# Optimization experiments

Measured on AMD Instinct MI355X. Metric: run time of the kernel, lower is better.

Reference implementation:

```python
import jax, jax.numpy as jnp
import numpy as np

D_MODEL = 1024
N_HEADS = 16
D_K = D_MODEL // N_HEADS


def setup_inputs() -> dict:
    key = jax.random.key(0)
    ks = jax.random.split(key, 11)
    B, S, D = 2, 2048, D_MODEL
    scale = 1.0 / np.sqrt(D)
    inp = {
        "q": jax.random.normal(ks[0], (B, S, D), jnp.float32),
        "k": jax.random.normal(ks[1], (B, S, D), jnp.float32),
        "v": jax.random.normal(ks[2], (B, S, D), jnp.float32),
        "wq": jax.random.normal(ks[3], (D, D), jnp.float32) * scale,
        "bq": jax.random.normal(ks[4], (D,), jnp.float32) * 0.01,
        "wk": jax.random.normal(ks[5], (D, D), jnp.float32) * scale,
        "bk": jax.random.normal(ks[6], (D,), jnp.float32) * 0.01,
        "wv": jax.random.normal(ks[7], (D, D), jnp.float32) * scale,
        "bv": jax.random.normal(ks[8], (D,), jnp.float32) * 0.01,
        "wo": jax.random.normal(ks[9], (D, D), jnp.float32) * scale,
        "bo": jax.random.normal(ks[10], (D,), jnp.float32) * 0.01,
    }
    return inp


def _split_heads(x, B):
    # [B, S, D] -> [B, H, S, d_k]
    return x.reshape(B, -1, N_HEADS, D_K).transpose(0, 2, 1, 3)


def reference(q, k, v, wq, bq, wk, bk, wv, bv, wo, bo):
    B, S, D = q.shape
    # Linear projections (torch Linear: x @ W^T + b)
    qh = _split_heads(q @ wq.T + bq, B)  # [B,H,S,dk]
    kh = _split_heads(k @ wk.T + bk, B)
    vh = _split_heads(v @ wv.T + bv, B)
    scores = jnp.einsum("bhqd,bhkd->bhqk", qh, kh) / jnp.sqrt(jnp.float32(D_K))
    attn = jax.nn.softmax(scores, axis=-1)  # [B,H,S,S]
    out = jnp.einsum("bhqk,bhkd->bhqd", attn, vh)  # [B,H,S,dk]
    out = out.transpose(0, 2, 1, 3).reshape(B, S, D)
    out = out @ wo.T + bo
    return (out, attn)
```

## Files before the change

### kernel.cpp

```cpp
#include <hip/hip_runtime.h>

#define D_MODEL 1024
#define N_HEADS 16
#define D_K     64
#define BB      2
#define SS      2048
#define M_TOT   (BB * SS)

typedef __attribute__((ext_vector_type(8))) short short8;
typedef __attribute__((ext_vector_type(4))) float f32x4;

__device__ __forceinline__ unsigned short bf_rne(float x) {
    unsigned u = __builtin_bit_cast(unsigned, x);
    u += 0x7fff + ((u >> 16) & 1);
    return (unsigned short)(u >> 16);
}
__device__ __forceinline__ void split2(float x, unsigned short& h, unsigned short& l) {
    unsigned short hh = bf_rne(x);
    float hf = __builtin_bit_cast(float, ((unsigned)hh) << 16);
    l = bf_rne(x - hf);
    h = hh;
}

__device__ __forceinline__ int swz(int r, int k) {
    return r * 64 + ((((k >> 3) ^ (r & 7)) << 3) | (k & 7));
}

__global__ __launch_bounds__(256) void split_f32(
    const float* __restrict__ in, unsigned short* __restrict__ h,
    unsigned short* __restrict__ l, int n4)
{
    int i = blockIdx.x * 256 + threadIdx.x;
    if (i >= n4) return;
    float4 v = ((const float4*)in)[i];
    unsigned short hh[4], ll[4];
    split2(v.x, hh[0], ll[0]); split2(v.y, hh[1], ll[1]);
    split2(v.z, hh[2], ll[2]); split2(v.w, hh[3], ll[3]);
    *(ushort4*)&h[i * 4] = make_ushort4(hh[0], hh[1], hh[2], hh[3]);
    *(ushort4*)&l[i * 4] = make_ushort4(ll[0], ll[1], ll[2], ll[3]);
}

template <int BN, int STORE, bool BIAS>
__global__ __launch_bounds__(256, 2) void gemm3(
    const float* __restrict__ A, long sAz, int lda,
    const unsigned short* __restrict__ Bh, const unsigned short* __restrict__ Bl,
    long sBz, int ldb,
    const float* __restrict__ bias,
    float* __restrict__ Cf, unsigned short* __restrict__ Ch,
    unsigned short* __restrict__ Cl,
    long sCz, int ldc, int K, float scale)
{
    constexpr int NF = (BN == 128) ? 4 : 2;
    constexpr int PB = BN / 32;

    const int z = blockIdx.z;
    A  += (long)z * sAz;
    Bh += (long)z * sBz;
    Bl += (long)z * sBz;

    const int m0 = blockIdx.y * 128;
    const int n0 = blockIdx.x * BN;
    const int t  = threadIdx.x;
    const int lane = t & 63;
    const int wy = t >> 7;
    const int wx = (t >> 6) & 1;

    __shared__ __align__(16) unsigned short Ahs[128 * 64];
    __shared__ __align__(16) unsigned short Als[128 * 64];
    __shared__ __align__(16) unsigned short Bhs[BN * 64];
    __shared__ __align__(16) unsigned short Bls[BN * 64];

    const int sr = t >> 3;
    const int sc = (t & 7) * 8;

    f32x4 acc[4][NF];
#pragma unroll
    for (int i = 0; i < 4; ++i)
#pragma unroll
        for (int j = 0; j < NF; ++j) acc[i][j] = (f32x4){0.f, 0.f, 0.f, 0.f};

    for (int k0 = 0; k0 < K; k0 += 64) {
        float4 a0[4], a1[4];
#pragma unroll
        for (int p = 0; p < 4; ++p) {
            const float* s = &A[(long)(m0 + sr + 32 * p) * lda + k0 + sc];
            a0[p] = *(const float4*)s;
            a1[p] = *(const float4*)(s + 4);
        }
        short8 gbh[PB], gbl[PB];
#pragma unroll
        for (int p = 0; p < PB; ++p) {
            const long bo = (long)(n0 + sr + 32 * p) * ldb + k0 + sc;
            gbh[p] = *(const short8*)&Bh[bo];
            gbl[p] = *(const short8*)&Bl[bo];
        }
        __syncthreads();
#pragma unroll
        for (int p = 0; p < 4; ++p) {
            union { short8 v; unsigned short u[8]; } ph, pl;
            float f[8] = {a0[p].x, a0[p].y, a0[p].z, a0[p].w,
                          a1[p].x, a1[p].y, a1[p].z, a1[p].w};
#pragma unroll
            for (int e = 0; e < 8; ++e) split2(f[e], ph.u[e], pl.u[e]);
            const int idx = swz(sr + 32 * p, sc);
            *(short8*)&Ahs[idx] = ph.v;
            *(short8*)&Als[idx] = pl.v;
        }
#pragma unroll
        for (int p = 0; p < PB; ++p) {
            const int idx = swz(sr + 32 * p, sc);
            *(short8*)&Bhs[idx] = gbh[p];
            *(short8*)&Bls[idx] = gbl[p];
        }
        __syncthreads();

#pragma unroll
        for (int ks = 0; ks < 2; ++ks) {
            const int fr = lane & 15;
            const int fk = ks * 32 + (lane >> 4) * 8;
            short8 ah[4], al[4], bh8[NF], bl8[NF];
#pragma unroll
            for (int i = 0; i < 4; ++i) {
                const int idx = swz(wy * 64 + i * 16 + fr, fk);
                ah[i] = *(const short8*)&Ahs[idx];
                al[i] = *(const short8*)&Als[idx];
            }
#pragma unroll
            for (int j = 0; j < NF; ++j) {
                const int idx = swz(wx * (16 * NF) + j * 16 + fr, fk);
                bh8[j] = *(const short8*)&Bhs[idx];
                bl8[j] = *(const short8*)&Bls[idx];
            }
#pragma unroll
            for (int i = 0; i < 4; ++i)
#pragma unroll
                for (int j = 0; j < NF; ++j) {
                    acc[i][j] = __builtin_amdgcn_mfma_f32_16x16x32_bf16(ah[i], bh8[j], acc[i][j], 0, 0, 0);
                    acc[i][j] = __builtin_amdgcn_mfma_f32_16x16x32_bf16(al[i], bh8[j], acc[i][j], 0, 0, 0);
                    acc[i][j] = __builtin_amdgcn_mfma_f32_16x16x32_bf16(ah[i], bl8[j], acc[i][j], 0, 0, 0);
                    acc[i][j] = __builtin_amdgcn_mfma_f32_16x16x32_bf16(al[i], bl8[j], acc[i][j], 0, 0, 0);
                }
        }
    }

    const int fr = lane & 15;
    const int fq = lane >> 4;
#pragma unroll
    for (int j = 0; j < NF; ++j) {
        const int n = n0 + wx * (16 * NF) + j * 16 + fr;
        const float bj = BIAS ? bias[n] : 0.0f;
#pragma unroll
        for (int i = 0; i < 4; ++i)
#pragma unroll
            for (int r = 0; r < 4; ++r) {
                const int m = m0 + wy * 64 + i * 16 + fq * 4 + r;
                const float val = acc[i][j][r] * scale + bj;
                if (STORE == 0) {
                    Cf[(long)z * sCz + (long)m * ldc + n] = val;
                } else if (STORE == 1) {
                    const int b = m >> 11, s = m & 2047, h = n >> 6, d = n & 63;
                    Cf[(((long)(b * N_HEADS + h)) * SS + s) * 64 + d] = val;
                } else if (STORE == 2) {
                    const int b = m >> 11, s = m & 2047, h = n >> 6, d = n & 63;
                    unsigned short hh, ll; split2(val, hh, ll);
                    const long idx = (((long)(b * N_HEADS + h)) * SS + s) * 64 + d;
                    Ch[idx] = hh; Cl[idx] = ll;
                } else if (STORE == 3) {
                    const int b = m >> 11, s = m & 2047, h = n >> 6, d = n & 63;
                    unsigned short hh, ll; split2(val, hh, ll);
                    const long idx = (((long)(b * N_HEADS + h)) * 64 + d) * SS + s;
                    Ch[idx] = hh; Cl[idx] = ll;
                } else {
                    const int b = z >> 4, h = z & 15;
                    Cf[((long)(b * SS + m)) * D_MODEL + h * 64 + n] = val;
                }
            }
    }
}

__global__ __launch_bounds__(256) void softmax_rows(float* __restrict__ attn)
{
    const long row = blockIdx.x;
    float* p = attn + row * (long)SS;
    const int t = threadIdx.x;

    float4 v0 = *(const float4*)&p[t * 4];
    float4 v1 = *(const float4*)&p[(t + 256) * 4];

    float m = fmaxf(fmaxf(fmaxf(v0.x, v0.y), fmaxf(v0.z, v0.w)),
                    fmaxf(fmaxf(v1.x, v1.y), fmaxf(v1.z, v1.w)));
#pragma unroll
    for (int off = 32; off >= 1; off >>= 1)
        m = fmaxf(m, __shfl_xor(m, off));

    __shared__ float red[8];
    if ((t & 63) == 0) red[t >> 6] = m;
    __syncthreads();
    m = fmaxf(fmaxf(red[0], red[1]), fmaxf(red[2], red[3]));

    v0.x = __expf(v0.x - m); v0.y = __expf(v0.y - m);
    v0.z = __expf(v0.z - m); v0.w = __expf(v0.w - m);
    v1.x = __expf(v1.x - m); v1.y = __expf(v1.y - m);
    v1.z = __expf(v1.z - m); v1.w = __expf(v1.w - m);

    float s = (v0.x + v0.y + v0.z + v0.w) + (v1.x + v1.y + v1.z + v1.w);
#pragma unroll
    for (int off = 32; off >= 1; off >>= 1)
        s += __shfl_xor(s, off);
    if ((t & 63) == 0) red[4 + (t >> 6)] = s;
    __syncthreads();
    s = (red[4] + red[5]) + (red[6] + red[7]);

    const float r = 1.0f / s;
    v0.x *= r; v0.y *= r; v0.z *= r; v0.w *= r;
    v1.x *= r; v1.y *= r; v1.z *= r; v1.w *= r;

    *(float4*)&p[t * 4] = v0;
    *(float4*)&p[(t + 256) * 4] = v1;
}

extern "C" void kernel_launch(void* const* d_in, const int* in_sizes, int n_in,
                              void* d_out, int out_size, void* d_ws, size_t ws_size,
                              hipStream_t stream)
{
    const float* q  = (const float*)d_in[0];
    const float* k  = (const float*)d_in[1];
    const float* v  = (const float*)d_in[2];
    const float* wq = (const float*)d_in[3];
    const float* bq = (const float*)d_in[4];
    const float* wk = (const float*)d_in[5];
    const float* bk = (const float*)d_in[6];
    const float* wv = (const float*)d_in[7];
    const float* bv = (const float*)d_in[8];
    const float* wo = (const float*)d_in[9];
    const float* bo = (const float*)d_in[10];

    float* out  = (float*)d_out;
    float* attn = out + (long)BB * SS * D_MODEL;

    char* ws = (char*)d_ws;
    float*          qh    = (float*)ws;
    unsigned short* kh_hi = (unsigned short*)(ws + (16L << 20));
    unsigned short* kh_lo = (unsigned short*)(ws + (24L << 20));
    unsigned short* vt_hi = (unsigned short*)(ws + (32L << 20));
    unsigned short* vt_lo = (unsigned short*)(ws + (40L << 20));
    float*          oh    = (float*)(ws + (48L << 20));
    unsigned short* wq_hi = (unsigned short*)(ws + (48L << 20));
    unsigned short* wq_lo = (unsigned short*)(ws + (50L << 20));
    unsigned short* wk_hi = (unsigned short*)(ws + (52L << 20));
    unsigned short* wk_lo = (unsigned short*)(ws + (54L << 20));
    unsigned short* wv_hi = (unsigned short*)(ws + (56L << 20));
    unsigned short* wv_lo = (unsigned short*)(ws + (58L << 20));
    unsigned short* wo_hi = (unsigned short*)(ws);
    unsigned short* wo_lo = (unsigned short*)(ws + (2L << 20));

    const dim3 blk(256);
    const int NW4 = (D_MODEL * D_MODEL) / 4;

    hipLaunchKernelGGL(split_f32, dim3(1024), blk, 0, stream, wq, wq_hi, wq_lo, NW4);
    hipLaunchKernelGGL(split_f32, dim3(1024), blk, 0, stream, wk, wk_hi, wk_lo, NW4);
    hipLaunchKernelGGL(split_f32, dim3(1024), blk, 0, stream, wv, wv_hi, wv_lo, NW4);

    const dim3 gproj(D_MODEL / 128, M_TOT / 128, 1);
    hipLaunchKernelGGL((gemm3<128, 1, true>), gproj, blk, 0, stream,
                       q, 0L, D_MODEL, wq_hi, wq_lo, 0L, D_MODEL, bq,
                       qh, (unsigned short*)nullptr, (unsigned short*)nullptr,
                       0L, 0, D_MODEL, 1.0f);
    hipLaunchKernelGGL((gemm3<128, 2, true>), gproj, blk, 0, stream,
                       k, 0L, D_MODEL, wk_hi, wk_lo, 0L, D_MODEL, bk,
                       (float*)nullptr, kh_hi, kh_lo, 0L, 0, D_MODEL, 1.0f);
    hipLaunchKernelGGL((gemm3<128, 3, true>), gproj, blk, 0, stream,
                       v, 0L, D_MODEL, wv_hi, wv_lo, 0L, D_MODEL, bv,
                       (float*)nullptr, vt_hi, vt_lo, 0L, 0, D_MODEL, 1.0f);

    const dim3 gsc(SS / 128, SS / 128, BB * N_HEADS);
    hipLaunchKernelGGL((gemm3<128, 0, false>), gsc, blk, 0, stream,
                       qh, (long)SS * 64, 64, kh_hi, kh_lo, (long)SS * 64, 64,
                       (const float*)nullptr,
                       attn, (unsigned short*)nullptr, (unsigned short*)nullptr,
                       (long)SS * SS, SS, D_K, 0.125f);

    hipLaunchKernelGGL(split_f32, dim3(1024), blk, 0, stream, wo, wo_hi, wo_lo, NW4);

    hipLaunchKernelGGL(softmax_rows, dim3(BB * N_HEADS * SS), blk, 0, stream, attn);

    const dim3 gpv(1, SS / 128, BB * N_HEADS);
    hipLaunchKernelGGL((gemm3<64, 4, false>), gpv, blk, 0, stream,
                       attn, (long)SS * SS, SS, vt_hi, vt_lo, (long)64 * SS, SS,
                       (const float*)nullptr,
                       oh, (unsigned short*)nullptr, (unsigned short*)nullptr,
                       0L, 0, SS, 1.0f);

    hipLaunchKernelGGL((gemm3<128, 0, true>), gproj, blk, 0, stream,
                       oh, 0L, D_MODEL, wo_hi, wo_lo, 0L, D_MODEL, bo,
                       out, (unsigned short*)nullptr, (unsigned short*)nullptr,
                       0L, D_MODEL, D_MODEL, 1.0f);
}
```

Before: 1.248 ms.

## Fuse QK^T, softmax and PV into one attention kernel; drop lo*lo MFMA term

Replaces the separate scores GEMM, row softmax kernel and PV GEMM with one fused kernel per (head, 128-row tile). It first computes scaled scores, writes them raw to the attn output and tracks an online row max and sum. It then re-reads the scores, normalizes them, writes the final probabilities back, and splits them to bf16 hi/lo for the PV MFMAs. Q is now stored as a bf16 hi/lo split, and the lo*lo MFMA term is dropped in all GEMMs, cutting matrix work by a quarter at a small cost in precision. The aim is to save launches and one full pass over the large attention matrix, at the cost of lower parallelism and a sequential two-phase schedule inside each block.

```diff
diff --git a/kernel.cpp b/kernel.cpp
--- a/kernel.cpp
+++ b/kernel.cpp
@@ -40,26 +40,18 @@
     *(ushort4*)&l[i * 4] = make_ushort4(ll[0], ll[1], ll[2], ll[3]);
 }
 
-template <int BN, int STORE, bool BIAS>
+template <int STORE, bool BIAS>
 __global__ __launch_bounds__(256, 2) void gemm3(
-    const float* __restrict__ A, long sAz, int lda,
+    const float* __restrict__ A, int lda,
     const unsigned short* __restrict__ Bh, const unsigned short* __restrict__ Bl,
-    long sBz, int ldb,
+    int ldb,
     const float* __restrict__ bias,
     float* __restrict__ Cf, unsigned short* __restrict__ Ch,
     unsigned short* __restrict__ Cl,
-    long sCz, int ldc, int K, float scale)
+    int ldc, int K)
 {
-    constexpr int NF = (BN == 128) ? 4 : 2;
-    constexpr int PB = BN / 32;
-
-    const int z = blockIdx.z;
-    A  += (long)z * sAz;
-    Bh += (long)z * sBz;
-    Bl += (long)z * sBz;
-
     const int m0 = blockIdx.y * 128;
-    const int n0 = blockIdx.x * BN;
+    const int n0 = blockIdx.x * 128;
     const int t  = threadIdx.x;
     const int lane = t & 63;
     const int wy = t >> 7;
@@ -67,17 +59,17 @@
 
     __shared__ __align__(16) unsigned short Ahs[128 * 64];
     __shared__ __align__(16) unsigned short Als[128 * 64];
-    __shared__ __align__(16) unsigned short Bhs[BN * 64];
-    __shared__ __align__(16) unsigned short Bls[BN * 64];
+    __shared__ __align__(16) unsigned short Bhs[128 * 64];
+    __shared__ __align__(16) unsigned short Bls[128 * 64];
 
     const int sr = t >> 3;
     const int sc = (t & 7) * 8;
 
-    f32x4 acc[4][NF];
+    f32x4 acc[4][4];
 #pragma unroll
     for (int i = 0; i < 4; ++i)
 #pragma unroll
-        for (int j = 0; j < NF; ++j) acc[i][j] = (f32x4){0.f, 0.f, 0.f, 0.f};
+        for (int j = 0; j < 4; ++j) acc[i][j] = (f32x4){0.f, 0.f, 0.f, 0.f};
 
     for (int k0 = 0; k0 < K; k0 += 64) {
         float4 a0[4], a1[4];
@@ -87,9 +79,9 @@
             a0[p] = *(const float4*)s;
             a1[p] = *(const float4*)(s + 4);
         }
-        short8 gbh[PB], gbl[PB];
-#pragma unroll
-        for (int p = 0; p < PB; ++p) {
+        short8 gbh[4], gbl[4];
+#pragma unroll
+        for (int p = 0; p < 4; ++p) {
             const long bo = (long)(n0 + sr + 32 * p) * ldb + k0 + sc;
             gbh[p] = *(const short8*)&Bh[bo];
             gbl[p] = *(const short8*)&Bl[bo];
@@ -105,10 +97,6 @@
             const int idx = swz(sr + 32 * p, sc);
             *(short8*)&Ahs[idx] = ph.v;
             *(short8*)&Als[idx] = pl.v;
-        }
-#pragma unroll
-        for (int p = 0; p < PB; ++p) {
-            const int idx = swz(sr + 32 * p, sc);
             *(short8*)&Bhs[idx] = gbh[p];
             *(short8*)&Bls[idx] = gbl[p];
         }
@@ -118,7 +106,7 @@
         for (int ks = 0; ks < 2; ++ks) {
             const int fr = lane & 15;
             const int fk = ks * 32 + (lane >> 4) * 8;
-            short8 ah[4], al[4], bh8[NF], bl8[NF];
+            short8 ah[4], al[4], bh8[4], bl8[4];
 #pragma unroll
             for (int i = 0; i < 4; ++i) {
                 const int idx = swz(wy * 64 + i * 16 + fr, fk);
@@ -126,19 +114,18 @@
                 al[i] = *(const short8*)&Als[idx];
             }
 #pragma unroll
-            for (int j = 0; j < NF; ++j) {
-                const int idx = swz(wx * (16 * NF) + j * 16 + fr, fk);
+            for (int j = 0; j < 4; ++j) {
+                const int idx = swz(wx * 64 + j * 16 + fr, fk);
                 bh8[j] = *(const short8*)&Bhs[idx];
                 bl8[j] = *(const short8*)&Bls[idx];
             }
 #pragma unroll
             for (int i = 0; i < 4; ++i)
 #pragma unroll
-                for (int j = 0; j < NF; ++j) {
+                for (int j = 0; j < 4; ++j) {
                     acc[i][j] = __builtin_amdgcn_mfma_f32_16x16x32_bf16(ah[i], bh8[j], acc[i][j], 0, 0, 0);
                     acc[i][j] = __builtin_amdgcn_mfma_f32_16x16x32_bf16(al[i], bh8[j], acc[i][j], 0, 0, 0);
                     acc[i][j] = __builtin_amdgcn_mfma_f32_16x16x32_bf16(ah[i], bl8[j], acc[i][j], 0, 0, 0);
-                    acc[i][j] = __builtin_amdgcn_mfma_f32_16x16x32_bf16(al[i], bl8[j], acc[i][j], 0, 0, 0);
                 }
         }
     }
@@ -146,77 +133,274 @@
     const int fr = lane & 15;
     const int fq = lane >> 4;
 #pragma unroll
-    for (int j = 0; j < NF; ++j) {
-        const int n = n0 + wx * (16 * NF) + j * 16 + fr;
+    for (int j = 0; j < 4; ++j) {
+        const int n = n0 + wx * 64 + j * 16 + fr;
         const float bj = BIAS ? bias[n] : 0.0f;
 #pragma unroll
         for (int i = 0; i < 4; ++i)
 #pragma unroll
             for (int r = 0; r < 4; ++r) {
                 const int m = m0 + wy * 64 + i * 16 + fq * 4 + r;
-                const float val = acc[i][j][r] * scale + bj;
+                const float val = acc[i][j][r] + bj;
                 if (STORE == 0) {
-                    Cf[(long)z * sCz + (long)m * ldc + n] = val;
-                } else if (STORE == 1) {
-                    const int b = m >> 11, s = m & 2047, h = n >> 6, d = n & 63;
-                    Cf[(((long)(b * N_HEADS + h)) * SS + s) * 64 + d] = val;
+                    Cf[(long)m * ldc + n] = val;
                 } else if (STORE == 2) {
                     const int b = m >> 11, s = m & 2047, h = n >> 6, d = n & 63;
                     unsigned short hh, ll; split2(val, hh, ll);
                     const long idx = (((long)(b * N_HEADS + h)) * SS + s) * 64 + d;
                     Ch[idx] = hh; Cl[idx] = ll;
-                } else if (STORE == 3) {
+                } else {
                     const int b = m >> 11, s = m & 2047, h = n >> 6, d = n & 63;
                     unsigned short hh, ll; split2(val, hh, ll);
                     const long idx = (((long)(b * N_HEADS + h)) * 64 + d) * SS + s;
                     Ch[idx] = hh; Cl[idx] = ll;
-                } else {
-                    const int b = z >> 4, h = z & 15;
-                    Cf[((long)(b * SS + m)) * D_MODEL + h * 64 + n] = val;
                 }
             }
     }
 }
 
-__global__ __launch_bounds__(256) void softmax_rows(float* __restrict__ attn)
+__global__ __launch_bounds__(256, 2) void attn_fused(
+    const unsigned short* __restrict__ qh_hi, const unsigned short* __restrict__ qh_lo,
+    const unsigned short* __restrict__ kh_hi, const unsigned short* __restrict__ kh_lo,
+    const unsigned short* __restrict__ vt_hi, const unsigned short* __restrict__ vt_lo,
+    float* __restrict__ attn, float* __restrict__ oh)
 {
-    const long row = blockIdx.x;
-    float* p = attn + row * (long)SS;
-    const int t = threadIdx.x;
-
-    float4 v0 = *(const float4*)&p[t * 4];
-    float4 v1 = *(const float4*)&p[(t + 256) * 4];
-
-    float m = fmaxf(fmaxf(fmaxf(v0.x, v0.y), fmaxf(v0.z, v0.w)),
-                    fmaxf(fmaxf(v1.x, v1.y), fmaxf(v1.z, v1.w)));
-#pragma unroll
-    for (int off = 32; off >= 1; off >>= 1)
-        m = fmaxf(m, __shfl_xor(m, off));
-
-    __shared__ float red[8];
-    if ((t & 63) == 0) red[t >> 6] = m;
+    const int z  = blockIdx.x;
+    const int m0 = blockIdx.y * 128;
+    const int b  = z >> 4;
+    const int h  = z & 15;
+    const int t  = threadIdx.x;
+    const int lane = t & 63;
+    const int wy = t >> 7;
+    const int wx = (t >> 6) & 1;
+    const int fr = lane & 15;
+    const int fg = lane >> 4;
+
+    __shared__ __align__(16) unsigned short Qh[128 * 64];
+    __shared__ __align__(16) unsigned short Ql[128 * 64];
+    __shared__ __align__(16) unsigned short Wh[128 * 64];
+    __shared__ __align__(16) unsigned short Wl[128 * 64];
+    __shared__ float red_m[2][128];
+    __shared__ float red_l[2][128];
+    __shared__ float sm_m[128];
+    __shared__ float sm_rl[128];
+
+    const int sr = t >> 3;
+    const int sc = (t & 7) * 8;
+
+    float* attnZ = attn + (long)z * SS * SS;
+
+#pragma unroll
+    for (int p = 0; p < 4; ++p) {
+        const long g = ((long)z * SS + m0 + sr + 32 * p) * 64 + sc;
+        *(short8*)&Qh[swz(sr + 32 * p, sc)] = *(const short8*)&qh_hi[g];
+        *(short8*)&Ql[swz(sr + 32 * p, sc)] = *(const short8*)&qh_lo[g];
+    }
+
+    float m_reg[16], l_reg[16];
+#pragma unroll
+    for (int e = 0; e < 16; ++e) { m_reg[e] = -3.0e38f; l_reg[e] = 0.f; }
+
+    for (int nt = 0; nt < 16; ++nt) {
+        const int j0 = nt * 128;
+        short8 kh8[4], kl8[4];
+#pragma unroll
+        for (int p = 0; p < 4; ++p) {
+            const long g = ((long)z * SS + j0 + sr + 32 * p) * 64 + sc;
+            kh8[p] = *(const short8*)&kh_hi[g];
+            kl8[p] = *(const short8*)&kh_lo[g];
+        }
+        __syncthreads();
+#pragma unroll
+        for (int p = 0; p < 4; ++p) {
+            const int idx = swz(sr + 32 * p, sc);
+            *(short8*)&Wh[idx] = kh8[p];
+            *(short8*)&Wl[idx] = kl8[p];
+        }
+        __syncthreads();
+
+        f32x4 acc[4][4];
+#pragma unroll
+        for (int i = 0; i < 4; ++i)
+#pragma unroll
+            for (int j = 0; j < 4; ++j) acc[i][j] = (f32x4){0.f, 0.f, 0.f, 0.f};
+
+#pragma unroll
+        for (int ks = 0; ks < 2; ++ks) {
+            const int fk = ks * 32 + fg * 8;
+            short8 ah[4], al[4], bh8[4], bl8[4];
+#pragma unroll
+            for (int i = 0; i < 4; ++i) {
+                const int idx = swz(wy * 64 + i * 16 + fr, fk);
+                ah[i] = *(const short8*)&Qh[idx];
+                al[i] = *(const short8*)&Ql[idx];
+            }
+#pragma unroll
+            for (int j = 0; j < 4; ++j) {
+                const int idx = swz(wx * 64 + j * 16 + fr, fk);
+                bh8[j] = *(const short8*)&Wh[idx];
+                bl8[j] = *(const short8*)&Wl[idx];
+            }
+#pragma unroll
+            for (int i = 0; i < 4; ++i)
+#pragma unroll
+                for (int j = 0; j < 4; ++j) {
+                    acc[i][j] = __builtin_amdgcn_mfma_f32_16x16x32_bf16(ah[i], bh8[j], acc[i][j], 0, 0, 0);
+                    acc[i][j] = __builtin_amdgcn_mfma_f32_16x16x32_bf16(al[i], bh8[j], acc[i][j], 0, 0, 0);
+                    acc[i][j] = __builtin_amdgcn_mfma_f32_16x16x32_bf16(ah[i], bl8[j], acc[i][j], 0, 0, 0);
+                }
+        }
+
+#pragma unroll
+        for (int i = 0; i < 4; ++i)
+#pragma unroll
+            for (int j = 0; j < 4; ++j) acc[i][j] *= 0.125f;
+
+#pragma unroll
+        for (int i = 0; i < 4; ++i)
+#pragma unroll
+            for (int r = 0; r < 4; ++r) {
+                const int e = i * 4 + r;
+                const float tmax = fmaxf(fmaxf(acc[i][0][r], acc[i][1][r]),
+                                         fmaxf(acc[i][2][r], acc[i][3][r]));
+                const float mO = m_reg[e];
+                const float mN = fmaxf(mO, tmax);
+                const float s = __expf(acc[i][0][r] - mN) + __expf(acc[i][1][r] - mN)
+                              + __expf(acc[i][2][r] - mN) + __expf(acc[i][3][r] - mN);
+                l_reg[e] = l_reg[e] * __expf(mO - mN) + s;
+                m_reg[e] = mN;
+            }
+
+#pragma unroll
+        for (int i = 0; i < 4; ++i)
+#pragma unroll
+            for (int r = 0; r < 4; ++r) {
+                const long row = (long)(m0 + wy * 64 + i * 16 + fg * 4 + r) * SS;
+#pragma unroll
+                for (int j = 0; j < 4; ++j)
+                    attnZ[row + j0 + wx * 64 + j * 16 + fr] = acc[i][j][r];
+            }
+    }
+
+#pragma unroll
+    for (int e = 0; e < 16; ++e) {
+        float mm = m_reg[e], ll = l_reg[e];
+#pragma unroll
+        for (int off = 1; off < 16; off <<= 1) {
+            const float mo = __shfl_xor(mm, off);
+            const float lo = __shfl_xor(ll, off);
+            const float M = fmaxf(mm, mo);
+            ll = ll * __expf(mm - M) + lo * __expf(mo - M);
+            mm = M;
+        }
+        m_reg[e] = mm; l_reg[e] = ll;
+    }
+    if (fr == 0) {
+#pragma unroll
+        for (int e = 0; e < 16; ++e) {
+            const int row = wy * 64 + (e >> 2) * 16 + fg * 4 + (e & 3);
+            red_m[wx][row] = m_reg[e];
+            red_l[wx][row] = l_reg[e];
+        }
+    }
     __syncthreads();
-    m = fmaxf(fmaxf(red[0], red[1]), fmaxf(red[2], red[3]));
-
-    v0.x = __expf(v0.x - m); v0.y = __expf(v0.y - m);
-    v0.z = __expf(v0.z - m); v0.w = __expf(v0.w - m);
-    v1.x = __expf(v1.x - m); v1.y = __expf(v1.y - m);
-    v1.z = __expf(v1.z - m); v1.w = __expf(v1.w - m);
-
-    float s = (v0.x + v0.y + v0.z + v0.w) + (v1.x + v1.y + v1.z + v1.w);
-#pragma unroll
-    for (int off = 32; off >= 1; off >>= 1)
-        s += __shfl_xor(s, off);
-    if ((t & 63) == 0) red[4 + (t >> 6)] = s;
+    if (t < 128) {
+        const float ma = red_m[0][t], mb = red_m[1][t];
+        const float M = fmaxf(ma, mb);
+        const float L = red_l[0][t] * __expf(ma - M) + red_l[1][t] * __expf(mb - M);
+        sm_m[t] = M;
+        sm_rl[t] = 1.0f / L;
+    }
     __syncthreads();
-    s = (red[4] + red[5]) + (red[6] + red[7]);
-
-    const float r = 1.0f / s;
-    v0.x *= r; v0.y *= r; v0.z *= r; v0.w *= r;
-    v1.x *= r; v1.y *= r; v1.z *= r; v1.w *= r;
-
-    *(float4*)&p[t * 4] = v0;
-    *(float4*)&p[(t + 256) * 4] = v1;
+
+    f32x4 oacc[4][2];
+#pragma unroll
+    for (int i = 0; i < 4; ++i)
+#pragma unroll
+        for (int j = 0; j < 2; ++j) oacc[i][j] = (f32x4){0.f, 0.f, 0.f, 0.f};
+
+    for (int k0 = 0; k0 < SS; k0 += 64) {
+        float4 a0[4], a1[4];
+#pragma unroll
+        for (int p = 0; p < 4; ++p) {
+            const float* src = &attnZ[(long)(m0 + sr + 32 * p) * SS + k0 + sc];
+            a0[p] = *(const float4*)src;
+            a1[p] = *(const float4*)(src + 4);
+        }
+        short8 vh8[2], vl8[2];
+#pragma unroll
+        for (int p = 0; p < 2; ++p) {
+            const long g = ((long)z * 64 + sr + 32 * p) * SS + k0 + sc;
+            vh8[p] = *(const short8*)&vt_hi[g];
+            vl8[p] = *(const short8*)&vt_lo[g];
+        }
+        __syncthreads();
+#pragma unroll
+        for (int p = 0; p < 4; ++p) {
+            const int rl_ = sr + 32 * p;
+            const float mR = sm_m[rl_], rR = sm_rl[rl_];
+            float f[8] = {a0[p].x, a0[p].y, a0[p].z, a0[p].w,
+                          a1[p].x, a1[p].y, a1[p].z, a1[p].w};
+            union { short8 v; unsigned short u[8]; } ph, pl;
+            float pv[8];
+#pragma unroll
+            for (int e = 0; e < 8; ++e) {
+                pv[e] = __expf(f[e] - mR) * rR;
+                split2(pv[e], ph.u[e], pl.u[e]);
+            }
+            float* dst = &attnZ[(long)(m0 + rl_) * SS + k0 + sc];
+            *(float4*)dst = make_float4(pv[0], pv[1], pv[2], pv[3]);
+            *(float4*)(dst + 4) = make_float4(pv[4], pv[5], pv[6], pv[7]);
+            const int idx = swz(rl_, sc);
+            *(short8*)&Wh[idx] = ph.v;
+            *(short8*)&Wl[idx] = pl.v;
+        }
+#pragma unroll
+        for (int p = 0; p < 2; ++p) {
+            const int idx = swz(sr + 32 * p, sc);
+            *(short8*)&Qh[idx] = vh8[p];
+            *(short8*)&Ql[idx] = vl8[p];
+        }
+        __syncthreads();
+
+#pragma unroll
+        for (int ks = 0; ks < 2; ++ks) {
+            const int fk = ks * 32 + fg * 8;
+            short8 pa_h[4], pa_l[4], vb_h[2], vb_l[2];
+#pragma unroll
+            for (int i = 0; i < 4; ++i) {
+                const int idx = swz(wy * 64 + i * 16 + fr, fk);
+                pa_h[i] = *(const short8*)&Wh[idx];
+                pa_l[i] = *(const short8*)&Wl[idx];
+            }
+#pragma unroll
+            for (int jn = 0; jn < 2; ++jn) {
+                const int idx = swz(wx * 32 + jn * 16 + fr, fk);
+                vb_h[jn] = *(const short8*)&Qh[idx];
+                vb_l[jn] = *(const short8*)&Ql[idx];
+            }
+#pragma unroll
+            for (int i = 0; i < 4; ++i)
+#pragma unroll
+                for (int jn = 0; jn < 2; ++jn) {
+                    oacc[i][jn] = __builtin_amdgcn_mfma_f32_16x16x32_bf16(pa_h[i], vb_h[jn], oacc[i][jn], 0, 0, 0);
+                    oacc[i][jn] = __builtin_amdgcn_mfma_f32_16x16x32_bf16(pa_l[i], vb_h[jn], oacc[i][jn], 0, 0, 0);
+                    oacc[i][jn] = __builtin_amdgcn_mfma_f32_16x16x32_bf16(pa_h[i], vb_l[jn], oacc[i][jn], 0, 0, 0);
+                }
+        }
+    }
+
+#pragma unroll
+    for (int jn = 0; jn < 2; ++jn) {
+        const int d = wx * 32 + jn * 16 + fr;
+#pragma unroll
+        for (int i = 0; i < 4; ++i)
+#pragma unroll
+            for (int r = 0; r < 4; ++r) {
+                const int m = m0 + wy * 64 + i * 16 + fg * 4 + r;
+                oh[((long)(b * SS + m)) * D_MODEL + h * 64 + d] = oacc[i][jn][r];
+            }
+    }
 }
 
 extern "C" void kernel_launch(void* const* d_in, const int* in_sizes, int n_in,
@@ -239,7 +423,8 @@
     float* attn = out + (long)BB * SS * D_MODEL;
 
     char* ws = (char*)d_ws;
-    float*          qh    = (float*)ws;
+    unsigned short* qh_hi = (unsigned short*)ws;
+    unsigned short* qh_lo = (unsigned short*)(ws + (8L  << 20));
     unsigned short* kh_hi = (unsigned short*)(ws + (16L << 20));
     unsigned short* kh_lo = (unsigned short*)(ws + (24L << 20));
     unsigned short* vt_hi = (unsigned short*)(ws + (32L << 20));
@@ -262,37 +447,23 @@
     hipLaunchKernelGGL(split_f32, dim3(1024), blk, 0, stream, wv, wv_hi, wv_lo, NW4);
 
     const dim3 gproj(D_MODEL / 128, M_TOT / 128, 1);
-    hipLaunchKernelGGL((gemm3<128, 1, true>), gproj, blk, 0, stream,
-                       q, 0L, D_MODEL, wq_hi, wq_lo, 0L, D_MODEL, bq,
-                       qh, (unsigned short*)nullptr, (unsigned short*)nullptr,
-                       0L, 0, D_MODEL, 1.0f);
-    hipLaunchKernelGGL((gemm3<128, 2, true>), gproj, blk, 0, stream,
-                       k, 0L, D_MODEL, wk_hi, wk_lo, 0L, D_MODEL, bk,
-                       (float*)nullptr, kh_hi, kh_lo, 0L, 0, D_MODEL, 1.0f);
-    hipLaunchKernelGGL((gemm3<128, 3, true>), gproj, blk, 0, stream,
-                       v, 0L, D_MODEL, wv_hi, wv_lo, 0L, D_MODEL, bv,
-                       (float*)nullptr, vt_hi, vt_lo, 0L, 0, D_MODEL, 1.0f);
-
-    const dim3 gsc(SS / 128, SS / 128, BB * N_HEADS);
-    hipLaunchKernelGGL((gemm3<128, 0, false>), gsc, blk, 0, stream,
-                       qh, (long)SS * 64, 64, kh_hi, kh_lo, (long)SS * 64, 64,
-                       (const float*)nullptr,
-                       attn, (unsigned short*)nullptr, (unsigned short*)nullptr,
-                       (long)SS * SS, SS, D_K, 0.125f);
+    hipLaunchKernelGGL((gemm3<2, true>), gproj, blk, 0, stream,
+                       q, D_MODEL, wq_hi, wq_lo, D_MODEL, bq,
+                       (float*)nullptr, qh_hi, qh_lo, 0, D_MODEL);
+    hipLaunchKernelGGL((gemm3<2, true>), gproj, blk, 0, stream,
+                       k, D_MODEL, wk_hi, wk_lo, D_MODEL, bk,
+                       (float*)nullptr, kh_hi, kh_lo, 0, D_MODEL);
+    hipLaunchKernelGGL((gemm3<3, true>), gproj, blk, 0, stream,
+                       v, D_MODEL, wv_hi, wv_lo, D_MODEL, bv,
+                       (float*)nullptr, vt_hi, vt_lo, 0, D_MODEL);
+
+    hipLaunchKernelGGL(attn_fused, dim3(BB * N_HEADS, SS / 128), blk, 0, stream,
+                       qh_hi, qh_lo, kh_hi, kh_lo, vt_hi, vt_lo, attn, oh);
 
     hipLaunchKernelGGL(split_f32, dim3(1024), blk, 0, stream, wo, wo_hi, wo_lo, NW4);
 
-    hipLaunchKernelGGL(softmax_rows, dim3(BB * N_HEADS * SS), blk, 0, stream, attn);
-
-    const dim3 gpv(1, SS / 128, BB * N_HEADS);
-    hipLaunchKernelGGL((gemm3<64, 4, false>), gpv, blk, 0, stream,
-                       attn, (long)SS * SS, SS, vt_hi, vt_lo, (long)64 * SS, SS,
-                       (const float*)nullptr,
-                       oh, (unsigned short*)nullptr, (unsigned short*)nullptr,
-                       0L, 0, SS, 1.0f);
-
-    hipLaunchKernelGGL((gemm3<128, 0, true>), gproj, blk, 0, stream,
-                       oh, 0L, D_MODEL, wo_hi, wo_lo, 0L, D_MODEL, bo,
+    hipLaunchKernelGGL((gemm3<0, true>), gproj, blk, 0, stream,
+                       oh, D_MODEL, wo_hi, wo_lo, D_MODEL, bo,
                        out, (unsigned short*)nullptr, (unsigned short*)nullptr,
-                       0L, D_MODEL, D_MODEL, 1.0f);
-}
+                       D_MODEL, D_MODEL);
+}
```

Measured after the change: 1.148 ms. 1.09x faster.
